# Performance work log

Hardware: AMD Instinct MI355X
Metric: run time of the kernel (lower is better)

The kernel has to match this reference:

```python
import jax, jax.numpy as jnp
import numpy as np

R_MAX = 5.0
NUM_BASIS = 8
CUTOFF_P = 6
N_LAYERS = 3
C = 64          # hidden_mul / channels of irreps_conv_out (64x0e+64x1o)
Z = 4           # element_number
AVG_DEG = 32.0  # num-neighbor normalization (E/N)
SQRT3 = 1.7320508075688772
SQRT2 = 1.4142135623730951


def _radial_embedding(r):
    # Bessel basis * polynomial cutoff (RadialEdgeEmbedding)
    rs = jnp.maximum(r, 1e-9)
    n = jnp.arange(1, NUM_BASIS + 1, dtype=r.dtype)  # (B,)
    bessel = jnp.sqrt(2.0 / R_MAX) * jnp.sin(n * jnp.pi * rs[:, None] / R_MAX) / rs[:, None]
    x = r / R_MAX
    p = float(CUTOFF_P)
    fc = (1.0
          - (p + 1.0) * (p + 2.0) / 2.0 * x ** CUTOFF_P
          + p * (p + 2.0) * x ** (CUTOFF_P + 1)
          - p * (p + 1.0) / 2.0 * x ** (CUTOFF_P + 2))
    fc = jnp.where(x < 1.0, fc, 0.0)
    return bessel * fc[:, None]  # (E, NUM_BASIS)


def setup_inputs() -> dict:
    key = jax.random.key(0)
    ks = jax.random.split(key, 20)
    N, E, B = 16000, 512000, 16
    atom_type = jax.random.randint(ks[0], (N,), 0, Z)
    # atoms in a 4A box so most edge lengths fall inside r_max=5
    atom_pos = jax.random.uniform(ks[1], (N, 3), dtype=jnp.float32) * 4.0
    edge_src = jax.random.randint(ks[2], (E,), 0, N)
    edge_dst = jax.random.randint(ks[3], (E,), 0, N)
    edge_cell_shift = jnp.zeros((E, 3), jnp.float32)
    cell = jnp.tile(jnp.eye(3, dtype=jnp.float32) * 10.0, (B, 1, 1)) \
        + 0.01 * jax.random.normal(ks[4], (B, 3, 3), jnp.float32)
    image_index = jax.random.randint(ks[5], (N,), 0, B)
    g = lambda k, s, fan: jax.random.normal(k, s, jnp.float32) / np.sqrt(fan)
    return {
        'atom_type': atom_type, 'atom_pos': atom_pos,
        'edge_src': edge_src, 'edge_dst': edge_dst,
        'edge_cell_shift': edge_cell_shift, 'cell': cell, 'image_index': image_index,
        'w_lin_in': g(ks[6], (Z, C), Z),
        'mlp_w1': g(ks[7], (N_LAYERS, NUM_BASIS, 64), NUM_BASIS),
        'mlp_b1': jnp.zeros((N_LAYERS, 64), jnp.float32),
        'mlp_w2': g(ks[8], (N_LAYERS, 64, 5 * C), 64),
        'w_self_s': g(ks[9], (N_LAYERS, C, C), C),
        'w_self_v': g(ks[10], (N_LAYERS, C, C), C),
        'w_gate': g(ks[11], (N_LAYERS, C, C), C),
        'w_lin1': g(ks[12], (C, 16), C),
        'w_lin2': g(ks[13], (16, 1), 16),
    }


def reference(atom_type, atom_pos, edge_src, edge_dst, edge_cell_shift, cell,
              image_index, w_lin_in, mlp_w1, mlp_b1, mlp_w2,
              w_self_s, w_self_v, w_gate, w_lin1, w_lin2):
    N = atom_pos.shape[0]
    # edge vectors with periodic cell shift
    edge_vec = atom_pos[edge_dst] - atom_pos[edge_src]
    edge_vec = edge_vec + jnp.einsum('ni,nij->nj', edge_cell_shift,
                                     cell.reshape(-1, 3, 3)[image_index[edge_src]])
    r = jnp.linalg.norm(edge_vec, axis=1)                      # (E,)
    unit = edge_vec / jnp.maximum(r, 1e-9)[:, None]
    # spherical harmonics lmax=1, component normalization: y0=1 (implicit), y1=sqrt(3)*unit
    y1 = SQRT3 * unit                                           # (E, 3)
    emb = _radial_embedding(r)                                  # (E, NUM_BASIS)

    # one-hot embedding + input linear (one-hot is all 0e -> scalar channels only)
    onehot = jax.nn.one_hot(atom_type, Z, dtype=atom_pos.dtype)
    s = onehot @ w_lin_in                                       # (N, C) l=0 features
    v = jnp.zeros((N, C, 3), atom_pos.dtype)                    # (N, C, 3) l=1 features

    inv_sqrt_deg = 1.0 / np.sqrt(AVG_DEG)
    for L in range(N_LAYERS):
        # radial MLP -> per-edge per-channel tensor-product path weights
        w = jax.nn.silu(emb @ mlp_w1[L] + mlp_b1[L]) @ mlp_w2[L]  # (E, 5C)
        w1, w2, w3, w4, w5 = jnp.split(w, 5, axis=1)              # (E, C) each
        s_src = s[edge_src]                                       # (E, C)
        v_src = v[edge_src]                                       # (E, C, 3)
        vdoty = jnp.einsum('ecx,ex->ec', v_src, y1)
        # CG tensor-product paths (l<=1):
        m_s = w1 * s_src + w2 * vdoty / SQRT3                     # 0x0->0, 1x1->0
        m_v = (w3[:, :, None] * s_src[:, :, None] * y1[:, None, :]      # 0x1->1
               + w4[:, :, None] * v_src                                  # 1x0->1
               + w5[:, :, None] * jnp.cross(v_src, y1[:, None, :]) / SQRT2)  # 1x1->1
        agg_s = jax.ops.segment_sum(m_s, edge_dst, num_segments=N) * inv_sqrt_deg
        agg_v = jax.ops.segment_sum(m_v, edge_dst, num_segments=N) * inv_sqrt_deg
        # gated self-interaction + resnet
        gate = jax.nn.sigmoid(agg_s @ w_gate[L])                  # (N, C)
        s = s + jax.nn.silu(agg_s @ w_self_s[L])
        v = v + jnp.einsum('ncx,cd->ndx', agg_v, w_self_v[L]) * gate[:, :, None]

    # o3.Linear to 16x0e then 1x0e (only scalar channels map to 0e outputs)
    atomic_energy = (s @ w_lin1) @ w_lin2                         # (N, 1)
    atomic_energy = atomic_energy * 1.0                           # atomic_scale
    return atomic_energy
```

## Files before the change

kernel.cpp:

```cpp
#include <hip/hip_runtime.h>
#include <hip/hip_fp16.h>
#include <math.h>

#define NUM_BASIS 8
#define SQRT3 1.7320508075688772f
#define SQRT2 1.4142135623730951f
#define INV_SQRT_DEG 0.17677669529663687f
#define PI_F 3.14159265358979323846f

typedef _Float16 half8 __attribute__((ext_vector_type(8)));
typedef float float4v __attribute__((ext_vector_type(4)));

__device__ __forceinline__ float sigmoidf_(float x) { return 1.0f / (1.0f + __expf(-x)); }
__device__ __forceinline__ float siluf_(float x) { return x * sigmoidf_(x); }

__device__ __forceinline__ void unp2(unsigned u, float& a, float& b) {
    __half2 h = *reinterpret_cast<__half2*>(&u);
    float2 f = __half22float2(h);
    a = f.x; b = f.y;
}
__device__ __forceinline__ unsigned pk2(float a, float b) {
    __half2 h = __floats2half2_rn(a, b);
    return *reinterpret_cast<unsigned*>(&h);
}

__global__ __launch_bounds__(256) void count_deg(
    const int* __restrict__ dst, int* __restrict__ deg, int E)
{
    int base = (blockIdx.x * blockDim.x + threadIdx.x) * 4;
    if (base + 3 < E) {
        int4 d4 = *(const int4*)(dst + base);
        atomicAdd(&deg[d4.x], 1);
        atomicAdd(&deg[d4.y], 1);
        atomicAdd(&deg[d4.z], 1);
        atomicAdd(&deg[d4.w], 1);
    } else {
        for (int e = base; e < E; e++) atomicAdd(&deg[dst[e]], 1);
    }
}

__global__ __launch_bounds__(1024) void scan_prep(
    const int* __restrict__ deg, int* __restrict__ cursor, int N,
    const float* __restrict__ W2, _Float16* __restrict__ w2f,
    const float* __restrict__ Wg, const float* __restrict__ Ws,
    const float* __restrict__ Wv, _Float16* __restrict__ wgtf,
    const float* __restrict__ Wl1, const float* __restrict__ Wl2,
    float* __restrict__ wl12)
{
    if (blockIdx.x != 0) {
        int idx = ((int)blockIdx.x - 1) * 1024 + (int)threadIdx.x;
        if (idx < 64) {
            float a = 0.f;
            #pragma unroll
            for (int j = 0; j < 16; j++) a = fmaf(Wl1[idx*16 + j], Wl2[j], a);
            wl12[idx] = a;
        }
        if (idx < 3 * 20480) {
            int L  = idx / 20480;
            int r  = idx % 20480;
            int cg = r / 5120;
            int r2 = r % 5120;
            int p  = r2 / 1024;
            int r3 = r2 % 1024;
            int kh = r3 / 512;
            int r4 = r3 % 512;
            int lane = r4 / 8;
            int j  = r4 % 8;
            int k = kh*32 + (lane >> 4)*8 + j;
            int n = p*64 + cg*16 + (lane & 15);
            float val = W2[(size_t)L*20480 + k*320 + n];
            if (p == 1)      val *= 0.5773502691896258f;
            else if (p == 4) val *= 0.7071067811865476f;
            w2f[idx] = (_Float16)val;
        } else if (idx < 3*20480 + 3*3*4096) {
            int idx2 = idx - 3*20480;
            int L   = idx2 / 12288;
            int rem = idx2 % 12288;
            int mat = rem / 4096;
            int r2  = rem % 4096;
            int cg  = r2 / 1024;
            int r3  = r2 % 1024;
            int kh  = r3 / 512;
            int r4  = r3 % 512;
            int lane = r4 / 8;
            int j   = r4 % 8;
            int k = kh*32 + (lane >> 4)*8 + j;
            int n = cg*16 + (lane & 15);
            const float* src = (mat == 0) ? Wg : (mat == 1) ? Ws : Wv;
            wgtf[idx2] = (_Float16)src[(size_t)L*4096 + k*64 + n];
        }
        return;
    }

    __shared__ int wsum[16];
    __shared__ int carry_s, tot_s;
    int tid = threadIdx.x;
    int wid = tid >> 6, lane = tid & 63;
    if (tid == 0) carry_s = 0;
    __syncthreads();
    for (int base = 0; base < N; base += 16384) {
        int i0 = base + tid * 16;
        int v[16];
        int sum = 0;
        #pragma unroll
        for (int k = 0; k < 16; k++) {
            int i = i0 + k;
            v[k] = (i < N) ? deg[i] : 0;
            sum += v[k];
        }
        int incl = sum;
        #pragma unroll
        for (int off = 1; off < 64; off <<= 1) {
            int t = __shfl_up(incl, off);
            if (lane >= off) incl += t;
        }
        if (lane == 63) wsum[wid] = incl;
        __syncthreads();
        if (wid == 0 && lane < 16) {
            int wv = wsum[lane];
            int wincl = wv;
            #pragma unroll
            for (int off = 1; off < 16; off <<= 1) {
                int t = __shfl_up(wincl, off);
                if (lane >= off) wincl += t;
            }
            wsum[lane] = wincl - wv;
            if (lane == 15) tot_s = wincl;
        }
        __syncthreads();
        int carry = carry_s;
        int run = carry + wsum[wid] + incl - sum;
        #pragma unroll
        for (int k = 0; k < 16; k++) {
            int i = i0 + k;
            if (i < N) cursor[i] = run;
            run += v[k];
        }
        __syncthreads();
        if (tid == 0) carry_s = carry + tot_s;
        __syncthreads();
    }
}

__global__ __launch_bounds__(256) void edge_pre_scatter(
    const float* __restrict__ pos, const int* __restrict__ src,
    const int* __restrict__ dst, const float* __restrict__ cs,
    const float* __restrict__ cell, const int* __restrict__ img,
    int* __restrict__ cursor, _Float16* __restrict__ emb,
    uint2* __restrict__ y14, int2* __restrict__ sdp, int E)
{
    int e = blockIdx.x * blockDim.x + threadIdx.x;
    if (e >= E) return;
    int si = src[e], di = dst[e];
    int slot = atomicAdd(&cursor[di], 1);
    sdp[slot] = make_int2(si, di);
    float vx = pos[di*3+0] - pos[si*3+0];
    float vy = pos[di*3+1] - pos[si*3+1];
    float vz = pos[di*3+2] - pos[si*3+2];
    float c0 = cs[(size_t)e*3+0], c1 = cs[(size_t)e*3+1], c2 = cs[(size_t)e*3+2];
    const float* M = cell + (size_t)img[si] * 9;
    vx += c0*M[0] + c1*M[3] + c2*M[6];
    vy += c0*M[1] + c1*M[4] + c2*M[7];
    vz += c0*M[2] + c1*M[5] + c2*M[8];
    float r  = sqrtf(vx*vx + vy*vy + vz*vz);
    float rs = fmaxf(r, 1e-9f);
    float inv = 1.0f / rs;
    uint2 yv;
    yv.x = pk2(SQRT3*vx*inv, SQRT3*vy*inv);
    yv.y = pk2(SQRT3*vz*inv, 0.f);
    y14[slot] = yv;
    float x = r * (1.0f / 5.0f);
    float x2 = x*x, x6 = x2*x2*x2;
    float fc = 1.0f - 28.0f*x6 + 48.0f*x6*x - 21.0f*x6*x2;
    if (x >= 1.0f) fc = 0.0f;
    float pre = sqrtf(2.0f / 5.0f) * inv * fc;
    float t = PI_F * rs * (1.0f / 5.0f);
    half8 ev;
    #pragma unroll
    for (int n = 1; n <= NUM_BASIS; n++)
        ev[n-1] = (_Float16)(pre * __sinf((float)n * t));
    *(half8*)(emb + (size_t)slot*NUM_BASIS) = ev;
}

__device__ __forceinline__ void mlp1_pre_body(
    const _Float16* __restrict__ emb, const float* __restrict__ W1,
    const float* __restrict__ B1, _Float16* __restrict__ hA, int E,
    int g, int nthreads)
{
    int kb   = (g & 7) * 8;
    int es   = g >> 3;
    int estr = nthreads >> 3;
    float wv[8][8];
    #pragma unroll
    for (int jj = 0; jj < 8; jj++) {
        float4 a = *(const float4*)(W1 + jj*64 + kb);
        float4 b = *(const float4*)(W1 + jj*64 + kb + 4);
        wv[jj][0]=a.x; wv[jj][1]=a.y; wv[jj][2]=a.z; wv[jj][3]=a.w;
        wv[jj][4]=b.x; wv[jj][5]=b.y; wv[jj][6]=b.z; wv[jj][7]=b.w;
    }
    float bv[8];
    {
        float4 a = *(const float4*)(B1 + kb);
        float4 b = *(const float4*)(B1 + kb + 4);
        bv[0]=a.x; bv[1]=a.y; bv[2]=a.z; bv[3]=a.w;
        bv[4]=b.x; bv[5]=b.y; bv[6]=b.z; bv[7]=b.w;
    }
    for (int e = es; e < E; e += estr) {
        half8 ev = *(const half8*)(emb + (size_t)e*8);
        float hv[8];
        #pragma unroll
        for (int j = 0; j < 8; j++) hv[j] = bv[j];
        #pragma unroll
        for (int jj = 0; jj < 8; jj++) {
            float em = (float)ev[jj];
            #pragma unroll
            for (int j = 0; j < 8; j++)
                hv[j] = fmaf(em, wv[jj][j], hv[j]);
        }
        half8 out;
        #pragma unroll
        for (int j = 0; j < 8; j++) out[j] = (_Float16)siluf_(hv[j]);
        *(half8*)(hA + (size_t)e*64 + kb) = out;
    }
}

__global__ __launch_bounds__(256) void mlp1_pre(
    const _Float16* __restrict__ emb, const float* __restrict__ W1,
    const float* __restrict__ B1, _Float16* __restrict__ hA, int E)
{
    int g = blockIdx.x * blockDim.x + threadIdx.x;
    mlp1_pre_body(emb, W1, B1, hA, E, g, gridDim.x * blockDim.x);
}

__device__ __forceinline__ void mlp1_afrag(
    const _Float16* __restrict__ emb, const float* __restrict__ W1,
    const float* __restrict__ B1, int eA, int q, half8 afrag[2])
{
    half8 ev = *(const half8*)(emb + (size_t)eA*8);
    float em[8];
    #pragma unroll
    for (int j = 0; j < 8; j++) em[j] = (float)ev[j];
    #pragma unroll
    for (int kh = 0; kh < 2; kh++) {
        int kb = kh*32 + q*8;
        float hv[8];
        float4 b0 = *(const float4*)(B1 + kb);
        float4 b1 = *(const float4*)(B1 + kb + 4);
        hv[0]=b0.x; hv[1]=b0.y; hv[2]=b0.z; hv[3]=b0.w;
        hv[4]=b1.x; hv[5]=b1.y; hv[6]=b1.z; hv[7]=b1.w;
        #pragma unroll
        for (int jj = 0; jj < 8; jj++) {
            float4 wa = *(const float4*)(W1 + jj*64 + kb);
            float4 wb = *(const float4*)(W1 + jj*64 + kb + 4);
            hv[0] = fmaf(em[jj], wa.x, hv[0]);
            hv[1] = fmaf(em[jj], wa.y, hv[1]);
            hv[2] = fmaf(em[jj], wa.z, hv[2]);
            hv[3] = fmaf(em[jj], wa.w, hv[3]);
            hv[4] = fmaf(em[jj], wb.x, hv[4]);
            hv[5] = fmaf(em[jj], wb.y, hv[5]);
            hv[6] = fmaf(em[jj], wb.z, hv[6]);
            hv[7] = fmaf(em[jj], wb.w, hv[7]);
        }
        #pragma unroll
        for (int j = 0; j < 8; j++)
            afrag[kh][j] = (_Float16)siluf_(hv[j]);
    }
}

template<bool PRE>
__global__ __launch_bounds__(256) void edge_msg_mfma_l0(
    const _Float16* __restrict__ emb, const _Float16* __restrict__ hA,
    const uint2* __restrict__ y14, const int2* __restrict__ sdp,
    const int* __restrict__ type, const float* __restrict__ wlin,
    const float* __restrict__ W1, const float* __restrict__ B1,
    const _Float16* __restrict__ w2f,
    float* __restrict__ aggs, float* __restrict__ aggx,
    float* __restrict__ aggy, float* __restrict__ aggz, int E)
{
    __shared__ _Float16 w2s[8192];
    {
        half8* dstv = (half8*)w2s;
        const half8* srcv = (const half8*)w2f;
        #pragma unroll
        for (int k = 0; k < 4; k++) {
            int t  = threadIdx.x + k*256;
            int cg = t >> 8;
            int r  = t & 255;
            int pp = r >> 7;
            int rk = r & 127;
            dstv[t] = srcv[cg*640 + pp*256 + rk];
        }
    }
    __syncthreads();

    int wave  = (blockIdx.x * blockDim.x + threadIdx.x) >> 6;
    int lane  = threadIdx.x & 63;
    int wbase = wave * 16;
    if (wbase >= E) return;
    int q   = lane >> 4;
    int col = lane & 15;

    half8 afrag[2];
    if (PRE) {
        const _Float16* hp = hA + (size_t)(wbase + col)*64 + q*8;
        afrag[0] = *(const half8*)(hp);
        afrag[1] = *(const half8*)(hp + 32);
    }

    int eb = wbase + q*4;
    int d[4], tt[4];
    float y1x[4], y1y[4], y1z[4];
    #pragma unroll
    for (int r = 0; r < 4; r++) {
        int2 sv = sdp[eb + r];
        tt[r] = type[sv.x];
        d[r]  = sv.y;
        uint2 yv = y14[eb + r];
        float dummy;
        unp2(yv.x, y1x[r], y1y[r]);
        unp2(yv.y, y1z[r], dummy);
    }

    if (!PRE) mlp1_afrag(emb, W1, B1, wbase + col, q, afrag);

    int dfirst = __shfl(d[0], 0);
    bool uni = __all(d[3] == dfirst);

    int dnq = __shfl_down(d[0], 16);
    int nd3 = (q == 3) ? -1 : dnq;
    int df = d[0], dl = d[3];
    bool U = (df == dl);
    int dlp = __shfl_up(dl, 16);
    bool link = (q > 0) && (dlp == df);

    #pragma unroll
    for (int cg = 0; cg < 4; cg++) {
        float4v a1 = {0,0,0,0}, a3 = {0,0,0,0};
        const _Float16* wbp = w2s + ((size_t)cg*2048) + (size_t)lane*8;
        {
            half8 b10 = *(const half8*)(wbp + 0*512);
            half8 b11 = *(const half8*)(wbp + 1*512);
            half8 b30 = *(const half8*)(wbp + 2*512);
            half8 b31 = *(const half8*)(wbp + 3*512);
            a1 = __builtin_amdgcn_mfma_f32_16x16x32_f16(afrag[0], b10, a1, 0, 0, 0);
            a1 = __builtin_amdgcn_mfma_f32_16x16x32_f16(afrag[1], b11, a1, 0, 0, 0);
            a3 = __builtin_amdgcn_mfma_f32_16x16x32_f16(afrag[0], b30, a3, 0, 0, 0);
            a3 = __builtin_amdgcn_mfma_f32_16x16x32_f16(afrag[1], b31, a3, 0, 0, 0);
        }
        int c = cg*16 + col;

        float ms[4], mx[4], my[4], mz[4];
        #pragma unroll
        for (int r = 0; r < 4; r++) {
            float s = wlin[tt[r]*64 + c];
            float w3s = a3[r] * s;
            ms[r] = a1[r] * s;
            mx[r] = w3s * y1x[r];
            my[r] = w3s * y1y[r];
            mz[r] = w3s * y1z[r];
        }

        if (uni) {
            float fs = (ms[0]+ms[1]) + (ms[2]+ms[3]);
            float fx = (mx[0]+mx[1]) + (mx[2]+mx[3]);
            float fy = (my[0]+my[1]) + (my[2]+my[3]);
            float fz = (mz[0]+mz[1]) + (mz[2]+mz[3]);
            fs += __shfl_xor(fs, 16); fx += __shfl_xor(fx, 16);
            fy += __shfl_xor(fy, 16); fz += __shfl_xor(fz, 16);
            fs += __shfl_xor(fs, 32); fx += __shfl_xor(fx, 32);
            fy += __shfl_xor(fy, 32); fz += __shfl_xor(fz, 32);
            if (q == 0) {
                size_t ai = (size_t)d[0]*64 + c;
                atomicAdd(aggs + ai, fs);
                atomicAdd(aggx + ai, fx);
                atomicAdd(aggy + ai, fy);
                atomicAdd(aggz + ai, fz);
            }
            continue;
        }

        #pragma unroll
        for (int r = 1; r < 4; r++) {
            if (d[r] == d[r-1]) {
                ms[r] += ms[r-1]; mx[r] += mx[r-1];
                my[r] += my[r-1]; mz[r] += mz[r-1];
            }
        }
        float Cs = 0.f, Cx = 0.f, Cy = 0.f, Cz = 0.f;
        #pragma unroll
        for (int it = 0; it < 3; it++) {
            float es = ms[3] + (U ? Cs : 0.f);
            float ex = mx[3] + (U ? Cx : 0.f);
            float ey = my[3] + (U ? Cy : 0.f);
            float ez = mz[3] + (U ? Cz : 0.f);
            float ts = __shfl_up(es, 16);
            float tx = __shfl_up(ex, 16);
            float ty = __shfl_up(ey, 16);
            float tz = __shfl_up(ez, 16);
            Cs = link ? ts : 0.f; Cx = link ? tx : 0.f;
            Cy = link ? ty : 0.f; Cz = link ? tz : 0.f;
        }
        bool hr = true;
        #pragma unroll
        for (int r = 0; r < 4; r++) {
            if (r > 0) hr = hr && (d[r] == d[r-1]);
            float fs = ms[r] + (hr ? Cs : 0.f);
            float fx = mx[r] + (hr ? Cx : 0.f);
            float fy = my[r] + (hr ? Cy : 0.f);
            float fz = mz[r] + (hr ? Cz : 0.f);
            int ndx = (r < 3) ? d[r+1] : nd3;
            if (ndx != d[r] && d[r] >= 0) {
                size_t ai = (size_t)d[r]*64 + c;
                atomicAdd(aggs + ai, fs);
                atomicAdd(aggx + ai, fx);
                atomicAdd(aggy + ai, fy);
                atomicAdd(aggz + ai, fz);
            }
        }
    }
}

__device__ __forceinline__ void process_half(
    const _Float16* __restrict__ w2s, const half8 afrag[2],
    const uint2 pf[4][2], const int d[4], int nd3, bool U, bool link,
    bool uni, bool live,
    const float* y1x, const float* y1y, const float* y1z,
    int cgh, int col,
    float* __restrict__ aggs, float* __restrict__ aggx,
    float* __restrict__ aggy, float* __restrict__ aggz)
{
    int lane = threadIdx.x & 63;
    int q = lane >> 4;
    #pragma unroll
    for (int cgl = 0; cgl < 2; cgl++) {
        float4v acc[5];
        #pragma unroll
        for (int p = 0; p < 5; p++) acc[p] = (float4v){0.f, 0.f, 0.f, 0.f};
        const _Float16* wbp = w2s + ((size_t)cgl*5120) + (size_t)lane*8;
        #pragma unroll
        for (int p = 0; p < 5; p++) {
            half8 bf0 = *(const half8*)(wbp + ((size_t)(p*2 + 0))*512);
            half8 bf1 = *(const half8*)(wbp + ((size_t)(p*2 + 1))*512);
            acc[p] = __builtin_amdgcn_mfma_f32_16x16x32_f16(afrag[0], bf0, acc[p], 0, 0, 0);
            acc[p] = __builtin_amdgcn_mfma_f32_16x16x32_f16(afrag[1], bf1, acc[p], 0, 0, 0);
        }
        int c = (cgh*2 + cgl)*16 + col;

        float ms[4], mx[4], my[4], mz[4];
        #pragma unroll
        for (int r = 0; r < 4; r++) {
            float fsx, fvx, fvy, fvz;
            unp2(pf[r][cgl].x, fsx, fvx);
            unp2(pf[r][cgl].y, fvy, fvz);
            float yx = y1x[r], yy = y1y[r], yz = y1z[r];
            float w1 = acc[0][r], w2 = acc[1][r], w3 = acc[2][r];
            float w4 = acc[3][r], w5 = acc[4][r];
            float vdoty = fvx*yx + fvy*yy + fvz*yz;
            ms[r] = fmaf(w1, fsx, w2*vdoty);
            float w3s = w3*fsx;
            float cx = fvy*yz - fvz*yy;
            float cy = fvz*yx - fvx*yz;
            float cz = fvx*yy - fvy*yx;
            mx[r] = fmaf(w3s, yx, fmaf(w4, fvx, w5*cx));
            my[r] = fmaf(w3s, yy, fmaf(w4, fvy, w5*cy));
            mz[r] = fmaf(w3s, yz, fmaf(w4, fvz, w5*cz));
        }

        if (uni) {
            float fs = (ms[0]+ms[1]) + (ms[2]+ms[3]);
            float fx = (mx[0]+mx[1]) + (mx[2]+mx[3]);
            float fy = (my[0]+my[1]) + (my[2]+my[3]);
            float fz = (mz[0]+mz[1]) + (mz[2]+mz[3]);
            fs += __shfl_xor(fs, 16); fx += __shfl_xor(fx, 16);
            fy += __shfl_xor(fy, 16); fz += __shfl_xor(fz, 16);
            fs += __shfl_xor(fs, 32); fx += __shfl_xor(fx, 32);
            fy += __shfl_xor(fy, 32); fz += __shfl_xor(fz, 32);
            if (q == 0 && live) {
                size_t ai = (size_t)d[0]*64 + c;
                atomicAdd(aggs + ai, fs);
                atomicAdd(aggx + ai, fx);
                atomicAdd(aggy + ai, fy);
                atomicAdd(aggz + ai, fz);
            }
            continue;
        }

        #pragma unroll
        for (int r = 1; r < 4; r++) {
            if (d[r] == d[r-1]) {
                ms[r] += ms[r-1]; mx[r] += mx[r-1];
                my[r] += my[r-1]; mz[r] += mz[r-1];
            }
        }
        float Cs = 0.f, Cx = 0.f, Cy = 0.f, Cz = 0.f;
        #pragma unroll
        for (int it = 0; it < 3; it++) {
            float es = ms[3] + (U ? Cs : 0.f);
            float ex = mx[3] + (U ? Cx : 0.f);
            float ey = my[3] + (U ? Cy : 0.f);
            float ez = mz[3] + (U ? Cz : 0.f);
            float ts = __shfl_up(es, 16);
            float tx = __shfl_up(ex, 16);
            float ty = __shfl_up(ey, 16);
            float tz = __shfl_up(ez, 16);
            Cs = link ? ts : 0.f; Cx = link ? tx : 0.f;
            Cy = link ? ty : 0.f; Cz = link ? tz : 0.f;
        }
        bool hr = true;
        #pragma unroll
        for (int r = 0; r < 4; r++) {
            if (r > 0) hr = hr && (d[r] == d[r-1]);
            float fs = ms[r] + (hr ? Cs : 0.f);
            float fx = mx[r] + (hr ? Cx : 0.f);
            float fy = my[r] + (hr ? Cy : 0.f);
            float fz = mz[r] + (hr ? Cz : 0.f);
            int ndx = (r < 3) ? d[r+1] : nd3;
            if (ndx != d[r] && d[r] >= 0 && live) {
                size_t ai = (size_t)d[r]*64 + c;
                atomicAdd(aggs + ai, fs);
                atomicAdd(aggx + ai, fx);
                atomicAdd(aggy + ai, fy);
                atomicAdd(aggz + ai, fz);
            }
        }
    }
}

template<bool PRE>
__global__ __launch_bounds__(256) void edge_msg_mfma(
    const _Float16* __restrict__ emb, const _Float16* __restrict__ hA,
    const uint2* __restrict__ y14, const int2* __restrict__ sdp,
    const uint2* __restrict__ nf,
    const float* __restrict__ W1, const float* __restrict__ B1,
    const _Float16* __restrict__ w2f,
    float* __restrict__ aggs, float* __restrict__ aggx,
    float* __restrict__ aggy, float* __restrict__ aggz, int E)
{
    __shared__ _Float16 w2s[10240];
    {
        half8* dstv = (half8*)w2s;
        const half8* srcv = (const half8*)w2f;
        #pragma unroll
        for (int k = 0; k < 5; k++)
            dstv[threadIdx.x + k*256] = srcv[threadIdx.x + k*256];
    }
    __syncthreads();

    int wave  = (blockIdx.x * blockDim.x + threadIdx.x) >> 6;
    int lane  = threadIdx.x & 63;
    int wbase = wave * 16;
    bool live = wbase < E;
    int wb2   = live ? wbase : 0;
    int q   = lane >> 4;
    int col = lane & 15;

    half8 afrag[2];
    if (PRE) {
        const _Float16* hp = hA + (size_t)(wb2 + col)*64 + q*8;
        afrag[0] = *(const half8*)(hp);
        afrag[1] = *(const half8*)(hp + 32);
    }

    int eb = wb2 + q*4;
    int d[4], si[4];
    float y1x[4], y1y[4], y1z[4];
    #pragma unroll
    for (int r = 0; r < 4; r++) {
        int2 sv = sdp[eb + r];
        si[r] = sv.x;
        d[r]  = sv.y;
        uint2 yv = y14[eb + r];
        float dummy;
        unp2(yv.x, y1x[r], y1y[r]);
        unp2(yv.y, y1z[r], dummy);
    }

    uint2 pf[4][2];
    #pragma unroll
    for (int r = 0; r < 4; r++) {
        size_t nb = (size_t)si[r] * 64 + col;
        pf[r][0] = nf[nb];
        pf[r][1] = nf[nb + 16];
    }

    if (!PRE) mlp1_afrag(emb, W1, B1, wb2 + col, q, afrag);

    int dfirst = __shfl(d[0], 0);
    bool uni = __all(d[3] == dfirst);

    int dnq = __shfl_down(d[0], 16);
    int nd3 = (q == 3) ? -1 : dnq;
    int df = d[0], dl = d[3];
    bool U = (df == dl);
    int dlp = __shfl_up(dl, 16);
    bool link = (q > 0) && (dlp == df);

    process_half(w2s, afrag, pf, d, nd3, U, link, uni, live,
                 y1x, y1y, y1z, 0, col, aggs, aggx, aggy, aggz);

    #pragma unroll
    for (int r = 0; r < 4; r++) {
        size_t nb = (size_t)si[r] * 64 + 32 + col;
        pf[r][0] = nf[nb];
        pf[r][1] = nf[nb + 16];
    }

    asm volatile("s_waitcnt lgkmcnt(0)" ::: "memory");
    __builtin_amdgcn_s_barrier();
    asm volatile("" ::: "memory");

    {
        half8* dstv = (half8*)w2s;
        const half8* srcv = (const half8*)w2f + 1280;
        #pragma unroll
        for (int k = 0; k < 5; k++)
            dstv[threadIdx.x + k*256] = srcv[threadIdx.x + k*256];
    }

    asm volatile("s_waitcnt lgkmcnt(0)" ::: "memory");
    __builtin_amdgcn_s_barrier();
    asm volatile("" ::: "memory");

    process_half(w2s, afrag, pf, d, nd3, U, link, uni, live,
                 y1x, y1y, y1z, 1, col, aggs, aggx, aggy, aggz);
}

__global__ __launch_bounds__(256) void node_update_mfma(
    uint2* __restrict__ nf,
    float* __restrict__ aggs, float* __restrict__ aggx,
    float* __restrict__ aggy, float* __restrict__ aggz,
    const _Float16* __restrict__ wgtf,
    const int* __restrict__ type, const float* __restrict__ wlin,
    const float* __restrict__ wl12,
    float* __restrict__ out, int first, int do_out, int N,
    const _Float16* __restrict__ emb, const float* __restrict__ W1n,
    const float* __restrict__ B1n, _Float16* __restrict__ hA, int E,
    int nb_node)
{
    if ((int)blockIdx.x >= nb_node) {
        int g = ((int)blockIdx.x - nb_node) * 256 + (int)threadIdx.x;
        mlp1_pre_body(emb, W1n, B1n, hA, E, g,
                      ((int)gridDim.x - nb_node) * 256);
        return;
    }

    __shared__ _Float16 wgs[12288];
    {
        half8* dstv = (half8*)wgs;
        const half8* srcv = (const half8*)wgtf;
        #pragma unroll
        for (int k = 0; k < 6; k++)
            dstv[threadIdx.x + k*256] = srcv[threadIdx.x + k*256];
    }

    int wave  = (blockIdx.x * blockDim.x + threadIdx.x) >> 6;
    int lane  = threadIdx.x & 63;
    int wbase = wave * 16;
    bool active = wbase < N;
    int q = lane >> 4, col = lane & 15;

    int nodeA = active ? (wbase + col) : 0;
    if (nodeA >= N) nodeA = N - 1;
    size_t nb = (size_t)nodeA * 64 + q * 8;
    half8 af0[2], af1[2], af2[2], af3[2];
    #pragma unroll
    for (int kh = 0; kh < 2; kh++) {
        const float* p0 = aggs + nb + kh*32;
        const float* p1 = aggx + nb + kh*32;
        const float* p2 = aggy + nb + kh*32;
        const float* p3 = aggz + nb + kh*32;
        float4 a0 = *(const float4*)p0, b0 = *(const float4*)(p0+4);
        float4 a1 = *(const float4*)p1, b1 = *(const float4*)(p1+4);
        float4 a2 = *(const float4*)p2, b2 = *(const float4*)(p2+4);
        float4 a3 = *(const float4*)p3, b3 = *(const float4*)(p3+4);
        af0[kh][0]=(_Float16)(a0.x*INV_SQRT_DEG); af0[kh][1]=(_Float16)(a0.y*INV_SQRT_DEG);
        af0[kh][2]=(_Float16)(a0.z*INV_SQRT_DEG); af0[kh][3]=(_Float16)(a0.w*INV_SQRT_DEG);
        af0[kh][4]=(_Float16)(b0.x*INV_SQRT_DEG); af0[kh][5]=(_Float16)(b0.y*INV_SQRT_DEG);
        af0[kh][6]=(_Float16)(b0.z*INV_SQRT_DEG); af0[kh][7]=(_Float16)(b0.w*INV_SQRT_DEG);
        af1[kh][0]=(_Float16)(a1.x*INV_SQRT_DEG); af1[kh][1]=(_Float16)(a1.y*INV_SQRT_DEG);
        af1[kh][2]=(_Float16)(a1.z*INV_SQRT_DEG); af1[kh][3]=(_Float16)(a1.w*INV_SQRT_DEG);
        af1[kh][4]=(_Float16)(b1.x*INV_SQRT_DEG); af1[kh][5]=(_Float16)(b1.y*INV_SQRT_DEG);
        af1[kh][6]=(_Float16)(b1.z*INV_SQRT_DEG); af1[kh][7]=(_Float16)(b1.w*INV_SQRT_DEG);
        af2[kh][0]=(_Float16)(a2.x*INV_SQRT_DEG); af2[kh][1]=(_Float16)(a2.y*INV_SQRT_DEG);
        af2[kh][2]=(_Float16)(a2.z*INV_SQRT_DEG); af2[kh][3]=(_Float16)(a2.w*INV_SQRT_DEG);
        af2[kh][4]=(_Float16)(b2.x*INV_SQRT_DEG); af2[kh][5]=(_Float16)(b2.y*INV_SQRT_DEG);
        af2[kh][6]=(_Float16)(b2.z*INV_SQRT_DEG); af2[kh][7]=(_Float16)(b2.w*INV_SQRT_DEG);
        af3[kh][0]=(_Float16)(a3.x*INV_SQRT_DEG); af3[kh][1]=(_Float16)(a3.y*INV_SQRT_DEG);
        af3[kh][2]=(_Float16)(a3.z*INV_SQRT_DEG); af3[kh][3]=(_Float16)(a3.w*INV_SQRT_DEG);
        af3[kh][4]=(_Float16)(b3.x*INV_SQRT_DEG); af3[kh][5]=(_Float16)(b3.y*INV_SQRT_DEG);
        af3[kh][6]=(_Float16)(b3.z*INV_SQRT_DEG); af3[kh][7]=(_Float16)(b3.w*INV_SQRT_DEG);
    }

    int tt[4];
    #pragma unroll
    for (int r = 0; r < 4; r++) {
        int nd = wbase + q*4 + r;
        tt[r] = type[(active && nd < N) ? nd : 0];
    }

    __syncthreads();

    float epart[4] = {0.f, 0.f, 0.f, 0.f};

    #pragma unroll
    for (int cg = 0; cg < 4; cg++) {
        const _Float16* bp = wgs + (size_t)lane * 8;
        half8 bg0 = *(const half8*)(bp + ((size_t)((0*4 + cg)*2 + 0))*512);
        half8 bg1 = *(const half8*)(bp + ((size_t)((0*4 + cg)*2 + 1))*512);
        half8 bs0 = *(const half8*)(bp + ((size_t)((1*4 + cg)*2 + 0))*512);
        half8 bs1 = *(const half8*)(bp + ((size_t)((1*4 + cg)*2 + 1))*512);
        half8 bv0 = *(const half8*)(bp + ((size_t)((2*4 + cg)*2 + 0))*512);
        half8 bv1 = *(const half8*)(bp + ((size_t)((2*4 + cg)*2 + 1))*512);
        float4v ag = {0,0,0,0}, as = {0,0,0,0};
        float4v ox = {0,0,0,0}, oy = {0,0,0,0}, oz = {0,0,0,0};
        ag = __builtin_amdgcn_mfma_f32_16x16x32_f16(af0[0], bg0, ag, 0, 0, 0);
        ag = __builtin_amdgcn_mfma_f32_16x16x32_f16(af0[1], bg1, ag, 0, 0, 0);
        as = __builtin_amdgcn_mfma_f32_16x16x32_f16(af0[0], bs0, as, 0, 0, 0);
        as = __builtin_amdgcn_mfma_f32_16x16x32_f16(af0[1], bs1, as, 0, 0, 0);
        ox = __builtin_amdgcn_mfma_f32_16x16x32_f16(af1[0], bv0, ox, 0, 0, 0);
        ox = __builtin_amdgcn_mfma_f32_16x16x32_f16(af1[1], bv1, ox, 0, 0, 0);
        oy = __builtin_amdgcn_mfma_f32_16x16x32_f16(af2[0], bv0, oy, 0, 0, 0);
        oy = __builtin_amdgcn_mfma_f32_16x16x32_f16(af2[1], bv1, oy, 0, 0, 0);
        oz = __builtin_amdgcn_mfma_f32_16x16x32_f16(af3[0], bv0, oz, 0, 0, 0);
        oz = __builtin_amdgcn_mfma_f32_16x16x32_f16(af3[1], bv1, oz, 0, 0, 0);

        if (!active) continue;
        int c = cg*16 + col;
        float wlc = wl12[c];
        #pragma unroll
        for (int r = 0; r < 4; r++) {
            int nd = wbase + q*4 + r;
            bool wr = nd < N;
            size_t ni = (size_t)nd*64 + c;
            float sx, vx, vy, vz;
            if (first) {
                sx = wlin[tt[r]*64 + c];
                vx = 0.f; vy = 0.f; vz = 0.f;
            } else {
                uint2 cur = nf[wr ? ni : 0];
                unp2(cur.x, sx, vx);
                unp2(cur.y, vy, vz);
            }
            float gate = sigmoidf_(ag[r]);
            sx += siluf_(as[r]);
            vx += ox[r] * gate;
            vy += oy[r] * gate;
            vz += oz[r] * gate;
            if (wr) {
                uint2 nv;
                nv.x = pk2(sx, vx);
                nv.y = pk2(vy, vz);
                nf[ni] = nv;
                aggs[ni] = 0.f;
                aggx[ni] = 0.f;
                aggy[ni] = 0.f;
                aggz[ni] = 0.f;
                epart[r] = fmaf(sx, wlc, epart[r]);
            }
        }
    }
    if (do_out && active) {
        #pragma unroll
        for (int r = 0; r < 4; r++) {
            float e = epart[r];
            e += __shfl_xor(e, 1);
            e += __shfl_xor(e, 2);
            e += __shfl_xor(e, 4);
            e += __shfl_xor(e, 8);
            int nd = wbase + q*4 + r;
            if (col == 0 && nd < N) out[nd] = e;
        }
    }
}

extern "C" void kernel_launch(void* const* d_in, const int* in_sizes, int n_in,
                              void* d_out, int out_size, void* d_ws, size_t ws_size,
                              hipStream_t stream)
{
    const int*   atom_type = (const int*)  d_in[0];
    const float* pos       = (const float*)d_in[1];
    const int*   src       = (const int*)  d_in[2];
    const int*   dst       = (const int*)  d_in[3];
    const float* cs        = (const float*)d_in[4];
    const float* cell      = (const float*)d_in[5];
    const int*   img       = (const int*)  d_in[6];
    const float* wlin_in   = (const float*)d_in[7];
    const float* mw1       = (const float*)d_in[8];
    const float* mb1       = (const float*)d_in[9];
    const float* mw2       = (const float*)d_in[10];
    const float* wss       = (const float*)d_in[11];
    const float* wsv       = (const float*)d_in[12];
    const float* wg        = (const float*)d_in[13];
    const float* wl1       = (const float*)d_in[14];
    const float* wl2       = (const float*)d_in[15];
    int N = in_sizes[0];
    int E = in_sizes[2];

    char* w = (char*)d_ws;
    _Float16* emb = (_Float16*)w; w += (size_t)E * 8 * sizeof(_Float16);
    uint2*  y14  = (uint2*)w;  w += (size_t)E * sizeof(uint2);
    int2*   sdp  = (int2*)w;   w += (size_t)E * sizeof(int2);
    uint2*  nf   = (uint2*)w;  w += (size_t)N * 64 * sizeof(uint2);
    float*  agg  = (float*)w;  w += (size_t)N * 64 * 4 * sizeof(float);
    _Float16* w2f  = (_Float16*)w; w += (size_t)3 * 20480 * sizeof(_Float16);
    _Float16* wgtf = (_Float16*)w; w += (size_t)3 * 3 * 4096 * sizeof(_Float16);
    float*  wl12 = (float*)w;  w += 64 * sizeof(float);
    int*    deg  = (int*)w;    w += (size_t)N * sizeof(int);
    int*    curs = (int*)w;    w += (size_t)N * sizeof(int);

    size_t used   = (size_t)(w - (char*)d_ws);
    size_t hbytes = (size_t)E * 64 * sizeof(_Float16);
    int nh = (ws_size >= used + hbytes) ? 1 : 0;
    _Float16* hbuf = (_Float16*)w;

    size_t NC = (size_t)N * 64;
    float* aggs = agg;
    float* aggx = agg + NC;
    float* aggy = agg + 2*NC;
    float* aggz = agg + 3*NC;

    hipMemsetAsync(deg, 0, (size_t)N * sizeof(int), stream);
    hipMemsetAsync(agg, 0, NC * 4 * sizeof(float), stream);
    count_deg<<<(E/4 + 255) / 256, 256, 0, stream>>>(dst, deg, E);
    int prep_n = 3*20480 + 3*3*4096;
    scan_prep<<<1 + (prep_n + 1023) / 1024, 1024, 0, stream>>>(
        deg, curs, N, mw2, w2f, wg, wss, wsv, wgtf, wl1, wl2, wl12);
    edge_pre_scatter<<<(E + 255) / 256, 256, 0, stream>>>(
        pos, src, dst, cs, cell, img, curs, emb, y14, sdp, E);

    int eblocks = (E + 63) / 64;
    int nblocks = (N + 63) / 64;
    int pblocks = 2048;

    if (nh) {
        mlp1_pre<<<pblocks, 256, 0, stream>>>(emb, mw1, mb1, hbuf, E);
        edge_msg_mfma_l0<true><<<eblocks, 256, 0, stream>>>(
            emb, hbuf, y14, sdp, atom_type, wlin_in,
            mw1, mb1, w2f, aggs, aggx, aggy, aggz, E);
    } else {
        edge_msg_mfma_l0<false><<<eblocks, 256, 0, stream>>>(
            emb, nullptr, y14, sdp, atom_type, wlin_in,
            mw1, mb1, w2f, aggs, aggx, aggy, aggz, E);
    }
    node_update_mfma<<<nblocks + (nh ? pblocks : 0), 256, 0, stream>>>(
        nf, aggs, aggx, aggy, aggz, wgtf, atom_type, wlin_in, wl12,
        (float*)d_out, 1, 0, N,
        emb, mw1 + 1 * 8 * 64, mb1 + 1 * 64, hbuf, E, nblocks);

    for (int L = 1; L < 3; L++) {
        if (nh) {
            edge_msg_mfma<true><<<eblocks, 256, 0, stream>>>(
                emb, hbuf, y14, sdp, nf,
                mw1 + L * 8 * 64, mb1 + L * 64, w2f + (size_t)L * 20480,
                aggs, aggx, aggy, aggz, E);
        } else {
            edge_msg_mfma<false><<<eblocks, 256, 0, stream>>>(
                emb, nullptr, y14, sdp, nf,
                mw1 + L * 8 * 64, mb1 + L * 64, w2f + (size_t)L * 20480,
                aggs, aggx, aggy, aggz, E);
        }
        int fuse = (nh && L < 2) ? pblocks : 0;
        node_update_mfma<<<nblocks + fuse, 256, 0, stream>>>(
            nf, aggs, aggx, aggy, aggz,
            wgtf + (size_t)L * 12288, atom_type, wlin_in, wl12,
            (float*)d_out, 0, (L == 2) ? 1 : 0, N,
            emb, mw1 + (L+1 < 3 ? L+1 : 0) * 8 * 64,
            mb1 + (L+1 < 3 ? L+1 : 0) * 64, hbuf, E,
            fuse ? nblocks : (nblocks + fuse + 1));
    }
}
```

Baseline: 450.0 us.

## Split edge message channel halves across wave pairs with full weight in LDS

The layer 1-2 edge message kernel now launches 512-thread blocks in which each pair of waves shares one 16-edge tile. Each wave handles one half of the channels, using a doubled LDS buffer that holds the whole W2 weight set. This removes the serial two-phase weight reload with its extra barriers and the per-wave sequential processing of both halves. The cost is duplicated edge-index loads and MLP A-fragment computation per wave pair, twice the LDS use per block, and possibly lower occupancy.

```diff
diff --git a/kernel.cpp b/kernel.cpp
--- a/kernel.cpp
+++ b/kernel.cpp
@@ -421,10 +421,9 @@
 }
 
 __device__ __forceinline__ void process_half(
-    const _Float16* __restrict__ w2s, const half8 afrag[2],
+    const _Float16* __restrict__ w2h, const half8 afrag[2],
     const uint2 pf[4][2], const int d[4], int nd3, bool U, bool link,
-    bool uni, bool live,
-    const float* y1x, const float* y1y, const float* y1z,
+    bool uni, const float* y1x, const float* y1y, const float* y1z,
     int cgh, int col,
     float* __restrict__ aggs, float* __restrict__ aggx,
     float* __restrict__ aggy, float* __restrict__ aggz)
@@ -436,7 +435,7 @@
         float4v acc[5];
         #pragma unroll
         for (int p = 0; p < 5; p++) acc[p] = (float4v){0.f, 0.f, 0.f, 0.f};
-        const _Float16* wbp = w2s + ((size_t)cgl*5120) + (size_t)lane*8;
+        const _Float16* wbp = w2h + ((size_t)cgl*5120) + (size_t)lane*8;
         #pragma unroll
         for (int p = 0; p < 5; p++) {
             half8 bf0 = *(const half8*)(wbp + ((size_t)(p*2 + 0))*512);
@@ -475,7 +474,7 @@
             fy += __shfl_xor(fy, 16); fz += __shfl_xor(fz, 16);
             fs += __shfl_xor(fs, 32); fx += __shfl_xor(fx, 32);
             fy += __shfl_xor(fy, 32); fz += __shfl_xor(fz, 32);
-            if (q == 0 && live) {
+            if (q == 0) {
                 size_t ai = (size_t)d[0]*64 + c;
                 atomicAdd(aggs + ai, fs);
                 atomicAdd(aggx + ai, fx);
@@ -515,7 +514,7 @@
             float fy = my[r] + (hr ? Cy : 0.f);
             float fz = mz[r] + (hr ? Cz : 0.f);
             int ndx = (r < 3) ? d[r+1] : nd3;
-            if (ndx != d[r] && d[r] >= 0 && live) {
+            if (ndx != d[r] && d[r] >= 0) {
                 size_t ai = (size_t)d[r]*64 + c;
                 atomicAdd(aggs + ai, fs);
                 atomicAdd(aggx + ai, fx);
@@ -527,7 +526,7 @@
 }
 
 template<bool PRE>
-__global__ __launch_bounds__(256) void edge_msg_mfma(
+__global__ __launch_bounds__(512) void edge_msg_mfma(
     const _Float16* __restrict__ emb, const _Float16* __restrict__ hA,
     const uint2* __restrict__ y14, const int2* __restrict__ sdp,
     const uint2* __restrict__ nf,
@@ -536,18 +535,20 @@
     float* __restrict__ aggs, float* __restrict__ aggx,
     float* __restrict__ aggy, float* __restrict__ aggz, int E)
 {
-    __shared__ _Float16 w2s[10240];
+    __shared__ _Float16 w2s[20480];
     {
         half8* dstv = (half8*)w2s;
         const half8* srcv = (const half8*)w2f;
         #pragma unroll
         for (int k = 0; k < 5; k++)
-            dstv[threadIdx.x + k*256] = srcv[threadIdx.x + k*256];
-    }
-    __syncthreads();
-
-    int wave  = (blockIdx.x * blockDim.x + threadIdx.x) >> 6;
-    int lane  = threadIdx.x & 63;
+            dstv[threadIdx.x + k*512] = srcv[threadIdx.x + k*512];
+    }
+
+    int widx = (int)threadIdx.x >> 6;
+    int pair = widx >> 1;
+    int h    = widx & 1;
+    int lane = threadIdx.x & 63;
+    int wave  = blockIdx.x * 4 + pair;
     int wbase = wave * 16;
     bool live = wbase < E;
     int wb2   = live ? wbase : 0;
@@ -578,7 +579,7 @@
     uint2 pf[4][2];
     #pragma unroll
     for (int r = 0; r < 4; r++) {
-        size_t nb = (size_t)si[r] * 64 + col;
+        size_t nb = (size_t)si[r] * 64 + h*32 + col;
         pf[r][0] = nf[nb];
         pf[r][1] = nf[nb + 16];
     }
@@ -595,34 +596,11 @@
     int dlp = __shfl_up(dl, 16);
     bool link = (q > 0) && (dlp == df);
 
-    process_half(w2s, afrag, pf, d, nd3, U, link, uni, live,
-                 y1x, y1y, y1z, 0, col, aggs, aggx, aggy, aggz);
-
-    #pragma unroll
-    for (int r = 0; r < 4; r++) {
-        size_t nb = (size_t)si[r] * 64 + 32 + col;
-        pf[r][0] = nf[nb];
-        pf[r][1] = nf[nb + 16];
-    }
-
-    asm volatile("s_waitcnt lgkmcnt(0)" ::: "memory");
-    __builtin_amdgcn_s_barrier();
-    asm volatile("" ::: "memory");
-
-    {
-        half8* dstv = (half8*)w2s;
-        const half8* srcv = (const half8*)w2f + 1280;
-        #pragma unroll
-        for (int k = 0; k < 5; k++)
-            dstv[threadIdx.x + k*256] = srcv[threadIdx.x + k*256];
-    }
-
-    asm volatile("s_waitcnt lgkmcnt(0)" ::: "memory");
-    __builtin_amdgcn_s_barrier();
-    asm volatile("" ::: "memory");
-
-    process_half(w2s, afrag, pf, d, nd3, U, link, uni, live,
-                 y1x, y1y, y1z, 1, col, aggs, aggx, aggy, aggz);
+    __syncthreads();
+    if (!live) return;
+
+    process_half(w2s + (size_t)h*10240, afrag, pf, d, nd3, U, link, uni,
+                 y1x, y1y, y1z, h, col, aggs, aggx, aggy, aggz);
 }
 
 __global__ __launch_bounds__(256) void node_update_mfma(
@@ -849,12 +827,12 @@
 
     for (int L = 1; L < 3; L++) {
         if (nh) {
-            edge_msg_mfma<true><<<eblocks, 256, 0, stream>>>(
+            edge_msg_mfma<true><<<eblocks, 512, 0, stream>>>(
                 emb, hbuf, y14, sdp, nf,
                 mw1 + L * 8 * 64, mb1 + L * 64, w2f + (size_t)L * 20480,
                 aggs, aggx, aggy, aggz, E);
         } else {
-            edge_msg_mfma<false><<<eblocks, 256, 0, stream>>>(
+            edge_msg_mfma<false><<<eblocks, 512, 0, stream>>>(
                 emb, nullptr, y14, sdp, nf,
                 mw1 + L * 8 * 64, mb1 + L * 64, w2f + (size_t)L * 20480,
                 aggs, aggx, aggy, aggz, E);
```

After: 466.7 us. 1.04x slower.
